# Performance work log

Hardware: AMD Instinct MI355X
Metric: run time of the kernel (lower is better)

## Reference

```python
import jax, jax.numpy as jnp
import numpy as np

B, S, D, H = 128, 512, 512, 4
DH = D // H

def setup_inputs() -> dict:
    key = jax.random.key(0)
    ks = jax.random.split(key, 12)
    s = 1.0 / np.sqrt(D)
    inp = {
        "x": jax.random.normal(ks[0], (B, S, D), dtype=jnp.float32),
        "Wi": jax.random.uniform(ks[1], (D, D), jnp.float32, -s, s),
        "bi": jnp.zeros((D,), jnp.float32),
        "Wq": jax.random.uniform(ks[2], (D, D), jnp.float32, -s, s),
        "bq": jnp.zeros((D,), jnp.float32),
        "Wk": jax.random.uniform(ks[3], (D, D), jnp.float32, -s, s),
        "bk": jnp.zeros((D,), jnp.float32),
        "Wv": jax.random.uniform(ks[4], (D, D), jnp.float32, -s, s),
        "bv": jnp.zeros((D,), jnp.float32),
        "Wo": jax.random.uniform(ks[5], (D, D), jnp.float32, -s, s),
        "bo": jnp.zeros((D,), jnp.float32),
        "data_lens": jax.random.randint(ks[6], (B,), 1, S + 1, dtype=jnp.int32),
    }
    return inp


def _forward(x, Wi, bi, Wq, bq, Wk, bk, Wv, bv, Wo, bo, data_lens):
    # fc_i applied to the whole sequence up front
    xf = x @ Wi + bi                      # [B, S, D]
    h0 = xf[:, 0, :]                      # initial state = fc_i(x)[:, 0]
    scale = 1.0 / jnp.sqrt(jnp.asarray(DH, xf.dtype))

    def step(h, x_t):
        # h: [B, D] previous state (acts as key and value, kv_len == 1)
        # x_t: [B, D] current input (query)
        q = (x_t @ Wq + bq).reshape(B, H, DH)
        k = (h @ Wk + bk).reshape(B, H, DH)
        v = (h @ Wv + bv).reshape(B, H, DH)
        scores = jnp.sum(q * k, axis=-1, keepdims=True) * scale   # [B, H, 1]
        w = jax.nn.softmax(scores, axis=-1)                       # == 1 (single key)
        attn = (w * v).reshape(B, D)
        h_new = attn @ Wo + bo + x_t                              # residual
        return h_new, h_new

    xs = jnp.transpose(xf, (1, 0, 2))     # [S, B, D]
    _, outs = jax.lax.scan(step, h0, xs)  # [S, B, D]
    outputs = jnp.transpose(outs, (1, 0, 2))                      # [B, S, D]

    idx = (data_lens.astype(jnp.int32) - 1)[:, None, None]        # [B,1,1]
    final_state = jnp.take_along_axis(outputs, idx, axis=1)[:, 0, :]
    return outputs, final_state


def reference(x, Wi, bi, Wq, bq, Wk, bk, Wv, bv, Wo, bo, data_lens):
    return _forward(x, Wi, bi, Wq, bq, Wk, bk, Wv, bv, Wo, bo, data_lens)
```

## Files before the change

### kernel.cpp

```cpp
#include <hip/hip_runtime.h>
#include <hip/hip_bf16.h>

typedef __hip_bfloat16 bf16;
typedef __attribute__((ext_vector_type(8))) short short8;
typedef __attribute__((ext_vector_type(4))) float f32x4;

#define S_LEN 512
#define DIM   512
#define BATCH 128
#define ROWS  (BATCH * S_LEN)

__device__ inline unsigned short f2bu(float f){
    bf16 h = __float2bfloat16(f);
    return *reinterpret_cast<unsigned short*>(&h);
}
__device__ inline float ld_in(const void* p, size_t i, int f32){
    return f32 ? ((const float*)p)[i] : __bfloat162float(((const bf16*)p)[i]);
}

__global__ void detect_dtype(const unsigned int* __restrict__ x, int* __restrict__ flag)
{
    __shared__ int cnt;
    if (threadIdx.x == 0) cnt = 0;
    __syncthreads();
    int loc = 0;
    for (int i = threadIdx.x; i < 8192; i += 256)
        if (((x[i] >> 7) & 0xFFu) == 0xFFu) loc++;
    atomicAdd(&cnt, loc);
    __syncthreads();
    if (threadIdx.x == 0) *flag = (cnt > 0) ? 1 : 0;
}

__global__ void conv_tr(const void* __restrict__ in, bf16* __restrict__ outp,
                        const int* __restrict__ flagp)
{
    const int f32 = *flagp;
    __shared__ unsigned short tile[32][33];
    const int bx = blockIdx.x, by = blockIdx.y;
    const int tx = threadIdx.x, ty = threadIdx.y;
    #pragma unroll
    for (int j = 0; j < 32; j += 8)
        tile[ty + j][tx] = f2bu(ld_in(in, (size_t)(by*32 + ty + j)*DIM + bx*32 + tx, f32));
    __syncthreads();
    #pragma unroll
    for (int j = 0; j < 32; j += 8) {
        unsigned short u = tile[tx][ty + j];
        outp[(size_t)(bx*32 + ty + j)*DIM + by*32 + tx] = *reinterpret_cast<bf16*>(&u);
    }
}

__global__ void conv_cp(const void* __restrict__ in, bf16* __restrict__ outp,
                        const int* __restrict__ flagp)
{
    const int f32 = *flagp;
    const size_t i = (size_t)blockIdx.x*256 + threadIdx.x;
    outp[i] = __float2bfloat16(ld_in(in, i, f32));
}

__global__ void cvec_kernel(const bf16* __restrict__ WoT, const void* __restrict__ bv,
                            const void* __restrict__ bo, const void* __restrict__ bi,
                            const int* __restrict__ flagp,
                            float* __restrict__ dvec, float* __restrict__ bvec)
{
    const int f32 = *flagp;
    const int n = threadIdx.x;
    float acc = 0.f;
    for (int k = 0; k < DIM; ++k)
        acc += ld_in(bv, k, f32) * __bfloat162float(WoT[(size_t)n*DIM + k]);
    const float dd = acc + ld_in(bo, n, f32);
    dvec[n] = dd;
    bvec[n] = dd + ld_in(bi, n, f32);
}

#define TILE_PROLOGUE                                                          \
    __shared__ __align__(16) unsigned short As[128][72];                       \
    __shared__ __align__(16) unsigned short Bs[128][72];                       \
    const int tid  = threadIdx.x;                                              \
    const int lane = tid & 63;                                                 \
    const int wave = tid >> 6;                                                 \
    const int wm = (wave & 1) * 64;                                            \
    const int wn = (wave >> 1) * 64;                                           \
    const int cn = lane & 15;                                                  \
    const int quad = lane >> 4;                                                \
    f32x4 acc[4][4];                                                           \
    _Pragma("unroll")                                                          \
    for (int i = 0; i < 4; ++i)                                                \
        _Pragma("unroll")                                                      \
        for (int j = 0; j < 4; ++j) acc[i][j] = (f32x4){0.f,0.f,0.f,0.f};

#define TILE_MFMA                                                              \
        __syncthreads();                                                       \
        _Pragma("unroll")                                                      \
        for (int ks = 0; ks < 64; ks += 32) {                                  \
            short8 af[4], bfr[4];                                              \
            const int koff = ks + quad*8;                                      \
            _Pragma("unroll")                                                  \
            for (int i = 0; i < 4; ++i) af[i]  = *(const short8*)&As[wm + i*16 + cn][koff]; \
            _Pragma("unroll")                                                  \
            for (int j = 0; j < 4; ++j) bfr[j] = *(const short8*)&Bs[wn + j*16 + cn][koff]; \
            _Pragma("unroll")                                                  \
            for (int i = 0; i < 4; ++i)                                        \
                _Pragma("unroll")                                              \
                for (int j = 0; j < 4; ++j)                                    \
                    acc[i][j] = __builtin_amdgcn_mfma_f32_16x16x32_bf16(af[i], bfr[j], acc[i][j], 0, 0, 0); \
        }                                                                      \
        __syncthreads();

#define STAGE_B(Bt, C0)                                                        \
        {                                                                      \
            int r = tid >> 3; const int c = (tid & 7) * 8;                     \
            _Pragma("unroll")                                                  \
            for (int p = 0; p < 4; ++p, r += 32) {                             \
                uint4 v = *(const uint4*)((Bt) + (size_t)((C0) + r)*DIM + k0 + c); \
                *(uint4*)&Bs[r][c] = v;                                        \
            }                                                                  \
        }

#define STAGE_A_IN(SRC, BASE)                                                  \
                if (f32) {                                                     \
                    const float* sp = (const float*)(SRC) + (BASE);            \
                    float4 a = *(const float4*)sp;                             \
                    float4 b = *(const float4*)(sp + 4);                       \
                    __align__(16) unsigned short w[8];                         \
                    w[0]=f2bu(a.x); w[1]=f2bu(a.y); w[2]=f2bu(a.z); w[3]=f2bu(a.w); \
                    w[4]=f2bu(b.x); w[5]=f2bu(b.y); w[6]=f2bu(b.z); w[7]=f2bu(b.w); \
                    *(uint4*)&As[r][c] = *(const uint4*)w;                     \
                } else {                                                       \
                    *(uint4*)&As[r][c] = *(const uint4*)((const bf16*)(SRC) + (BASE)); \
                }

__global__ __launch_bounds__(256) void gemm_sq(const bf16* __restrict__ A,
        const bf16* __restrict__ Btm, bf16* __restrict__ Pout, bf16* __restrict__ Tout)
{
    TILE_PROLOGUE
    const int R0 = blockIdx.y * 128;
    const int C0 = blockIdx.x * 128;
    for (int k0 = 0; k0 < DIM; k0 += 64) {
        {
            int r = tid >> 3; const int c = (tid & 7) * 8;
            #pragma unroll
            for (int p = 0; p < 4; ++p, r += 32)
                *(uint4*)&As[r][c] = *(const uint4*)(A + (size_t)(R0 + r)*DIM + k0 + c);
        }
        STAGE_B(Btm, C0)
        TILE_MFMA
    }
    #pragma unroll
    for (int i = 0; i < 4; ++i) {
        const int rowb = R0 + wm + i*16 + quad*4;
        #pragma unroll
        for (int j = 0; j < 4; ++j) {
            const int cc = C0 + wn + j*16 + cn;
            #pragma unroll
            for (int rr = 0; rr < 4; ++rr) {
                const float v = acc[i][j][rr];
                Pout[(size_t)(rowb + rr)*DIM + cc] = __float2bfloat16(v);
                Tout[(size_t)cc*DIM + rowb + rr]  = __float2bfloat16(v);
            }
        }
    }
}

__global__ __launch_bounds__(256) void gemm_xf_chunk(const void* __restrict__ X,
        size_t eoff, const bf16* __restrict__ WiT, const float* __restrict__ bvec,
        const int* __restrict__ flagp, float* __restrict__ U)
{
    const int f32 = *flagp;
    TILE_PROLOGUE
    const int R0 = blockIdx.y * 128;
    const int C0 = blockIdx.x * 128;
    for (int k0 = 0; k0 < DIM; k0 += 64) {
        {
            int r = tid >> 3; const int c = (tid & 7) * 8;
            #pragma unroll
            for (int p = 0; p < 4; ++p, r += 32) {
                const size_t base = eoff + (size_t)(R0 + r)*DIM + k0 + c;
                STAGE_A_IN(X, base)
            }
        }
        STAGE_B(WiT, C0)
        TILE_MFMA
    }
    #pragma unroll
    for (int i = 0; i < 4; ++i) {
        const int rowb = R0 + wm + i*16 + quad*4;
        #pragma unroll
        for (int j = 0; j < 4; ++j) {
            const int cc = C0 + wn + j*16 + cn;
            const float bb = bvec[cc];
            #pragma unroll
            for (int rr = 0; rr < 4; ++rr)
                U[(size_t)(rowb + rr)*DIM + cc] = acc[i][j][rr] + bb;
        }
    }
}

__global__ __launch_bounds__(256) void gemm_row0(const void* __restrict__ X,
        const bf16* __restrict__ WiT, const float* __restrict__ bvec,
        const int* __restrict__ flagp, float* __restrict__ U0)
{
    const int f32 = *flagp;
    TILE_PROLOGUE
    const int C0 = blockIdx.x * 128;
    for (int k0 = 0; k0 < DIM; k0 += 64) {
        {
            int r = tid >> 3; const int c = (tid & 7) * 8;
            #pragma unroll
            for (int p = 0; p < 4; ++p, r += 32) {
                const size_t base = (size_t)r*S_LEN*DIM + k0 + c;
                STAGE_A_IN(X, base)
            }
        }
        STAGE_B(WiT, C0)
        TILE_MFMA
    }
    #pragma unroll
    for (int i = 0; i < 4; ++i) {
        const int rowb = wm + i*16 + quad*4;
        #pragma unroll
        for (int j = 0; j < 4; ++j) {
            const int cc = C0 + wn + j*16 + cn;
            const float bb = bvec[cc];
            #pragma unroll
            for (int rr = 0; rr < 4; ++rr)
                U0[(size_t)(rowb + rr)*DIM + cc] = acc[i][j][rr] + bb;
        }
    }
}

__global__ __launch_bounds__(256) void gemm_v0(const float* __restrict__ U0,
        const bf16* __restrict__ T0, const float* __restrict__ dvec, float* __restrict__ V0)
{
    TILE_PROLOGUE
    const int C0 = blockIdx.x * 128;
    for (int k0 = 0; k0 < DIM; k0 += 64) {
        {
            int r = tid >> 3; const int c = (tid & 7) * 8;
            #pragma unroll
            for (int p = 0; p < 4; ++p, r += 32) {
                __align__(16) unsigned short w[8];
                #pragma unroll
                for (int q = 0; q < 8; ++q)
                    w[q] = f2bu(U0[(size_t)r*DIM + k0 + c + q] - dvec[k0 + c + q]);
                *(uint4*)&As[r][c] = *(const uint4*)w;
            }
        }
        STAGE_B(T0, C0)
        TILE_MFMA
    }
    #pragma unroll
    for (int i = 0; i < 4; ++i) {
        const int rowb = wm + i*16 + quad*4;
        #pragma unroll
        for (int j = 0; j < 4; ++j) {
            const int cc = C0 + wn + j*16 + cn;
            #pragma unroll
            for (int rr = 0; rr < 4; ++rr) {
                const size_t off = (size_t)(rowb + rr)*DIM + cc;
                V0[off] = acc[i][j][rr] + U0[off];
            }
        }
    }
}

template<bool TO_OUT>
__global__ __launch_bounds__(256) void gemm_level(const float* __restrict__ yin,
        void* __restrict__ yout, size_t eoff, const bf16* __restrict__ Bt,
        const float* __restrict__ dvec, const float* __restrict__ V0c,
        const int* __restrict__ flagp, const int shift, const int mode)
{
    const int f32 = *flagp;
    TILE_PROLOGUE
    const int R0 = blockIdx.y * 128;
    const int C0 = blockIdx.x * 128;
    for (int k0 = 0; k0 < DIM; k0 += 64) {
        {
            int r = tid >> 3; const int c = (tid & 7) * 8;
            #pragma unroll
            for (int p = 0; p < 4; ++p, r += 32) {
                const int row = R0 + r;
                const int t = row & (S_LEN - 1);
                __align__(16) unsigned short w[8];
                if (mode && t == 1) {
                    const float* vp = V0c + (size_t)(row >> 9)*DIM + k0 + c;
                    #pragma unroll
                    for (int q = 0; q < 8; ++q) w[q] = f2bu(vp[q]);
                } else if (mode && t == 0) {
                    const float* sp = yin + (size_t)row*DIM + k0 + c;
                    #pragma unroll
                    for (int q = 0; q < 8; ++q) w[q] = f2bu(sp[q] - dvec[k0 + c + q]);
                } else if (t >= shift) {
                    const float* sp = yin + (size_t)(row - shift)*DIM + k0 + c;
                    #pragma unroll
                    for (int q = 0; q < 8; ++q) w[q] = f2bu(sp[q]);
                } else {
                    #pragma unroll
                    for (int q = 0; q < 8; ++q) w[q] = 0;
                }
                *(uint4*)&As[r][c] = *(const uint4*)w;
            }
        }
        STAGE_B(Bt, C0)
        TILE_MFMA
    }
    #pragma unroll
    for (int i = 0; i < 4; ++i) {
        const int rowb = R0 + wm + i*16 + quad*4;
        #pragma unroll
        for (int j = 0; j < 4; ++j) {
            const int cc = C0 + wn + j*16 + cn;
            #pragma unroll
            for (int rr = 0; rr < 4; ++rr) {
                const size_t off = (size_t)(rowb + rr)*DIM + cc;
                const float v = acc[i][j][rr] + yin[off];
                if (TO_OUT) {
                    if (f32) ((float*)yout)[eoff + off] = v;
                    else     ((bf16*)yout)[eoff + off] = __float2bfloat16(v);
                } else {
                    ((float*)yout)[off] = v;
                }
            }
        }
    }
}

__global__ void gather_final(void* __restrict__ out, const int* __restrict__ lens,
                             const int* __restrict__ flagp)
{
    const int f32 = *flagp;
    const int idx = blockIdx.x * 256 + threadIdx.x;
    const int b = idx >> 9, n = idx & 511;
    int L = lens[b];
    if (L < 1) L = 1;
    if (L > S_LEN) L = S_LEN;
    const size_t src = ((size_t)b*S_LEN + (L - 1))*DIM + n;
    const size_t dst = (size_t)ROWS*DIM + idx;
    if (f32) ((float*)out)[dst] = ((const float*)out)[src];
    else     ((bf16*)out)[dst]  = ((const bf16*)out)[src];
}

extern "C" void kernel_launch(void* const* d_in, const int* in_sizes, int n_in,
                              void* d_out, int out_size, void* d_ws, size_t ws_size,
                              hipStream_t stream)
{
    const void* X  = d_in[0];
    const void* Wi = d_in[1];
    const void* bi = d_in[2];
    const void* Wv = d_in[7];
    const void* bv = d_in[8];
    const void* Wo = d_in[9];
    const void* bo = d_in[10];
    const int* lens = (const int*)d_in[11];
    char* ws = (char*)d_ws;

    const size_t MATB = (size_t)DIM * DIM * sizeof(bf16);
    bf16* WiT = (bf16*)(ws + 0*MATB);
    bf16* WoT = (bf16*)(ws + 1*MATB);
    bf16* Wvb = (bf16*)(ws + 2*MATB);
    bf16* S2  = (bf16*)(ws + 3*MATB);
    bf16* S3  = (bf16*)(ws + 4*MATB);
    bf16* T0  = (bf16*)(ws + 5*MATB);
    bf16* T1  = (bf16*)(ws + 6*MATB);
    bf16* T2  = (bf16*)(ws + 7*MATB);
    bf16* T3  = (bf16*)(ws + 8*MATB);
    float* dvec = (float*)(ws + 9*MATB);
    float* bvec = dvec + DIM;
    int*   flag = (int*)(bvec + DIM);
    float* U0   = (float*)(flag + 64);
    float* V0   = U0 + (size_t)BATCH*DIM;
    char*  dyn  = (char*)(V0 + (size_t)BATCH*DIM);
    const size_t fixed = (size_t)(dyn - ws);
    const size_t avail = ws_size > fixed ? ws_size - fixed : 0;

    int CR = 512;
    for (int cr = 65536; cr >= 512; cr >>= 1)
        if ((size_t)2*cr*DIM*4 <= avail) { CR = cr; break; }

    detect_dtype<<<1, 256, 0, stream>>>((const unsigned int*)X, flag);
    conv_tr<<<dim3(16,16), dim3(32,8), 0, stream>>>(Wi, WiT, flag);
    conv_tr<<<dim3(16,16), dim3(32,8), 0, stream>>>(Wo, WoT, flag);
    conv_cp<<<1024, 256, 0, stream>>>(Wv, Wvb, flag);
    cvec_kernel<<<1, DIM, 0, stream>>>(WoT, bv, bo, bi, flag, dvec, bvec);
    gemm_sq<<<dim3(4,4), 256, 0, stream>>>(Wvb, WoT, S2, T0);
    gemm_sq<<<dim3(4,4), 256, 0, stream>>>(S2, T0, S3, T1);
    gemm_sq<<<dim3(4,4), 256, 0, stream>>>(S3, T1, S2, T2);
    gemm_sq<<<dim3(4,4), 256, 0, stream>>>(S2, T2, S3, T3);
    gemm_row0<<<dim3(4,1), 256, 0, stream>>>(X, WiT, bvec, flag, U0);
    gemm_v0<<<dim3(4,1), 256, 0, stream>>>(U0, T0, dvec, V0);

    float* bufA = (float*)dyn;
    float* bufB = bufA + (size_t)CR*DIM;
    const int NC = ROWS / CR;
    const int RT = CR / 128;
    for (int c = 0; c < NC; ++c) {
        const size_t eoff = (size_t)c*CR*DIM;
        const float* V0c = V0 + (size_t)(c*(CR/S_LEN))*DIM;
        gemm_xf_chunk<<<dim3(4,RT), 256, 0, stream>>>(X, eoff, WiT, bvec, flag, bufA);
        gemm_level<false><<<dim3(4,RT), 256, 0, stream>>>(bufA, bufB, 0, T0, dvec, V0c, flag, 1, 1);
        gemm_level<false><<<dim3(4,RT), 256, 0, stream>>>(bufB, bufA, 0, T1, dvec, V0c, flag, 2, 0);
        gemm_level<false><<<dim3(4,RT), 256, 0, stream>>>(bufA, bufB, 0, T2, dvec, V0c, flag, 4, 0);
        gemm_level<true ><<<dim3(4,RT), 256, 0, stream>>>(bufB, d_out, eoff, T3, dvec, V0c, flag, 8, 0);
    }
    gather_final<<<256, 256, 0, stream>>>(d_out, lens, flag);
}
```

Measured before the change: 1.144 ms.

## Stage GEMM operands as bf16 via direct global-to-LDS loads

Replaces the per-level GEMM kernels with a unified gemm_big. Its A operand is a bf16 copy written by the previous level, and both tiles are staged through global_load_lds 16-byte loads into unpadded LDS. Input x is converted to bf16 by a separate pass, row-0/row-1 special cases are precomputed into small bf16 arrays, and block indices are swizzled for L2 locality. This removes the per-element fp32 load, convert and store to LDS in the inner loop, at the cost of extra bf16 writes per level and unpadded LDS rows that may cause bank conflicts. cvec is also parallelised with wave reductions.

```diff
diff --git a/kernel.cpp b/kernel.cpp
--- a/kernel.cpp
+++ b/kernel.cpp
@@ -16,6 +16,12 @@
 }
 __device__ inline float ld_in(const void* p, size_t i, int f32){
     return f32 ? ((const float*)p)[i] : __bfloat162float(((const bf16*)p)[i]);
+}
+
+typedef __attribute__((address_space(1))) const unsigned int gu32;
+typedef __attribute__((address_space(3))) unsigned int lu32;
+__device__ __forceinline__ void gld16(const void* g, void* l){
+    __builtin_amdgcn_global_load_lds((gu32*)g, (lu32*)l, 16, 0, 0);
 }
 
 __global__ void detect_dtype(const unsigned int* __restrict__ x, int* __restrict__ flag)
@@ -57,19 +63,53 @@
     outp[i] = __float2bfloat16(ld_in(in, i, f32));
 }
 
+__global__ void conv_x(const void* __restrict__ X, size_t eoff, bf16* __restrict__ xb,
+                       const int* __restrict__ flagp)
+{
+    const int f32 = *flagp;
+    const size_t i = ((size_t)blockIdx.x*256 + threadIdx.x)*8;
+    if (f32) {
+        const float* p = (const float*)X + eoff + i;
+        float4 a = *(const float4*)p;
+        float4 b = *(const float4*)(p + 4);
+        __align__(16) unsigned short wv[8];
+        wv[0]=f2bu(a.x); wv[1]=f2bu(a.y); wv[2]=f2bu(a.z); wv[3]=f2bu(a.w);
+        wv[4]=f2bu(b.x); wv[5]=f2bu(b.y); wv[6]=f2bu(b.z); wv[7]=f2bu(b.w);
+        *(uint4*)(xb + i) = *(const uint4*)wv;
+    } else {
+        *(uint4*)(xb + i) = *(const uint4*)((const bf16*)X + eoff + i);
+    }
+}
+
 __global__ void cvec_kernel(const bf16* __restrict__ WoT, const void* __restrict__ bv,
                             const void* __restrict__ bo, const void* __restrict__ bi,
                             const int* __restrict__ flagp,
                             float* __restrict__ dvec, float* __restrict__ bvec)
 {
     const int f32 = *flagp;
-    const int n = threadIdx.x;
+    const int n = blockIdx.x * 4 + (threadIdx.x >> 6);
+    const int lane = threadIdx.x & 63;
     float acc = 0.f;
-    for (int k = 0; k < DIM; ++k)
+    for (int k = lane; k < DIM; k += 64)
         acc += ld_in(bv, k, f32) * __bfloat162float(WoT[(size_t)n*DIM + k]);
-    const float dd = acc + ld_in(bo, n, f32);
-    dvec[n] = dd;
-    bvec[n] = dd + ld_in(bi, n, f32);
+    #pragma unroll
+    for (int o = 32; o > 0; o >>= 1) acc += __shfl_down(acc, o, 64);
+    if (lane == 0) {
+        const float dd = acc + ld_in(bo, n, f32);
+        dvec[n] = dd;
+        bvec[n] = dd + ld_in(bi, n, f32);
+    }
+}
+
+__global__ void prep_aux(const float* __restrict__ U0, const float* __restrict__ V0,
+                         const float* __restrict__ dvec,
+                         bf16* __restrict__ A1, bf16* __restrict__ V0b, bf16* __restrict__ Zr)
+{
+    const int idx = blockIdx.x * 256 + threadIdx.x;
+    const int n = idx & 511;
+    A1[idx]  = __float2bfloat16(U0[idx] - dvec[n]);
+    V0b[idx] = __float2bfloat16(V0[idx]);
+    if (idx < 512) Zr[idx] = __float2bfloat16(0.f);
 }
 
 #define TILE_PROLOGUE                                                          \
@@ -161,40 +201,6 @@
     }
 }
 
-__global__ __launch_bounds__(256) void gemm_xf_chunk(const void* __restrict__ X,
-        size_t eoff, const bf16* __restrict__ WiT, const float* __restrict__ bvec,
-        const int* __restrict__ flagp, float* __restrict__ U)
-{
-    const int f32 = *flagp;
-    TILE_PROLOGUE
-    const int R0 = blockIdx.y * 128;
-    const int C0 = blockIdx.x * 128;
-    for (int k0 = 0; k0 < DIM; k0 += 64) {
-        {
-            int r = tid >> 3; const int c = (tid & 7) * 8;
-            #pragma unroll
-            for (int p = 0; p < 4; ++p, r += 32) {
-                const size_t base = eoff + (size_t)(R0 + r)*DIM + k0 + c;
-                STAGE_A_IN(X, base)
-            }
-        }
-        STAGE_B(WiT, C0)
-        TILE_MFMA
-    }
-    #pragma unroll
-    for (int i = 0; i < 4; ++i) {
-        const int rowb = R0 + wm + i*16 + quad*4;
-        #pragma unroll
-        for (int j = 0; j < 4; ++j) {
-            const int cc = C0 + wn + j*16 + cn;
-            const float bb = bvec[cc];
-            #pragma unroll
-            for (int rr = 0; rr < 4; ++rr)
-                U[(size_t)(rowb + rr)*DIM + cc] = acc[i][j][rr] + bb;
-        }
-    }
-}
-
 __global__ __launch_bounds__(256) void gemm_row0(const void* __restrict__ X,
         const bf16* __restrict__ WiT, const float* __restrict__ bvec,
         const int* __restrict__ flagp, float* __restrict__ U0)
@@ -263,46 +269,86 @@
     }
 }
 
-template<bool TO_OUT>
-__global__ __launch_bounds__(256) void gemm_level(const float* __restrict__ yin,
-        void* __restrict__ yout, size_t eoff, const bf16* __restrict__ Bt,
-        const float* __restrict__ dvec, const float* __restrict__ V0c,
-        const int* __restrict__ flagp, const int shift, const int mode)
-{
-    const int f32 = *flagp;
-    TILE_PROLOGUE
-    const int R0 = blockIdx.y * 128;
-    const int C0 = blockIdx.x * 128;
+template<int MODE, bool TO_OUT>
+__global__ __launch_bounds__(256) void gemm_big(
+        const bf16* __restrict__ Abf, const bf16* __restrict__ A1,
+        const bf16* __restrict__ V0b, const bf16* __restrict__ Zr,
+        const bf16* __restrict__ Bt,  const float* __restrict__ Rf,
+        float* __restrict__ Of, bf16* __restrict__ Ob,
+        void* __restrict__ Oout, size_t eoff, const int* __restrict__ flagp,
+        const int shift)
+{
+    __shared__ __align__(16) unsigned short As[128*64];
+    __shared__ __align__(16) unsigned short Bs[128*64];
+    const int tid  = threadIdx.x;
+    const int lane = tid & 63;
+    const int w    = tid >> 6;
+    const int nb = gridDim.x;
+    const int p0 = blockIdx.x;
+    const int L  = (p0 & 7) * (nb >> 3) + (p0 >> 3);
+    const int bx = L & 3, by = L >> 2;
+    const int R0 = by * 128, C0 = bx * 128;
+    const int wm = (w & 1) * 64;
+    const int wn = (w >> 1) * 64;
+    const int cn = lane & 15;
+    const int quad = lane >> 4;
+    f32x4 acc[4][4];
+    #pragma unroll
+    for (int i = 0; i < 4; ++i)
+        #pragma unroll
+        for (int j = 0; j < 4; ++j) acc[i][j] = (f32x4){0.f,0.f,0.f,0.f};
+
+    const int lr = lane >> 3;
+    const int lc = (lane & 7) * 8;
+    const bf16* ab[4];
+    const bf16* bb[4];
+    #pragma unroll
+    for (int p = 0; p < 4; ++p) {
+        const int seg  = w*4 + p;
+        const int r    = seg*8 + lr;
+        const int grow = R0 + r;
+        const bf16* a;
+        if (MODE == 2) {
+            a = Abf + (size_t)grow*DIM;
+        } else if (MODE == 1) {
+            const int t = grow & (S_LEN - 1);
+            if      (t == 0) a = A1  + (size_t)(grow >> 9)*DIM;
+            else if (t == 1) a = V0b + (size_t)(grow >> 9)*DIM;
+            else             a = Abf + (size_t)(grow - 1)*DIM;
+        } else {
+            const int t = grow & (S_LEN - 1);
+            a = (t >= shift) ? (Abf + (size_t)(grow - shift)*DIM) : Zr;
+        }
+        ab[p] = a + lc;
+        bb[p] = Bt + (size_t)(C0 + r)*DIM + lc;
+    }
+
     for (int k0 = 0; k0 < DIM; k0 += 64) {
-        {
-            int r = tid >> 3; const int c = (tid & 7) * 8;
-            #pragma unroll
-            for (int p = 0; p < 4; ++p, r += 32) {
-                const int row = R0 + r;
-                const int t = row & (S_LEN - 1);
-                __align__(16) unsigned short w[8];
-                if (mode && t == 1) {
-                    const float* vp = V0c + (size_t)(row >> 9)*DIM + k0 + c;
-                    #pragma unroll
-                    for (int q = 0; q < 8; ++q) w[q] = f2bu(vp[q]);
-                } else if (mode && t == 0) {
-                    const float* sp = yin + (size_t)row*DIM + k0 + c;
-                    #pragma unroll
-                    for (int q = 0; q < 8; ++q) w[q] = f2bu(sp[q] - dvec[k0 + c + q]);
-                } else if (t >= shift) {
-                    const float* sp = yin + (size_t)(row - shift)*DIM + k0 + c;
-                    #pragma unroll
-                    for (int q = 0; q < 8; ++q) w[q] = f2bu(sp[q]);
-                } else {
-                    #pragma unroll
-                    for (int q = 0; q < 8; ++q) w[q] = 0;
-                }
-                *(uint4*)&As[r][c] = *(const uint4*)w;
-            }
-        }
-        STAGE_B(Bt, C0)
-        TILE_MFMA
-    }
+        #pragma unroll
+        for (int p = 0; p < 4; ++p) {
+            const int seg = w*4 + p;
+            gld16(ab[p] + k0, &As[seg*512]);
+            gld16(bb[p] + k0, &Bs[seg*512]);
+        }
+        __syncthreads();
+        #pragma unroll
+        for (int ks = 0; ks < 64; ks += 32) {
+            short8 af[4], bfr[4];
+            const int koff = ks + quad*8;
+            #pragma unroll
+            for (int i = 0; i < 4; ++i) af[i]  = *(const short8*)&As[(wm + i*16 + cn)*64 + koff];
+            #pragma unroll
+            for (int j = 0; j < 4; ++j) bfr[j] = *(const short8*)&Bs[(wn + j*16 + cn)*64 + koff];
+            #pragma unroll
+            for (int i = 0; i < 4; ++i)
+                #pragma unroll
+                for (int j = 0; j < 4; ++j)
+                    acc[i][j] = __builtin_amdgcn_mfma_f32_16x16x32_bf16(af[i], bfr[j], acc[i][j], 0, 0, 0);
+        }
+        __syncthreads();
+    }
+
+    const int f32o = TO_OUT ? *flagp : 0;
     #pragma unroll
     for (int i = 0; i < 4; ++i) {
         const int rowb = R0 + wm + i*16 + quad*4;
@@ -312,12 +358,14 @@
             #pragma unroll
             for (int rr = 0; rr < 4; ++rr) {
                 const size_t off = (size_t)(rowb + rr)*DIM + cc;
-                const float v = acc[i][j][rr] + yin[off];
+                const float res = (MODE == 2) ? Rf[cc] : Rf[off];
+                const float v = acc[i][j][rr] + res;
                 if (TO_OUT) {
-                    if (f32) ((float*)yout)[eoff + off] = v;
-                    else     ((bf16*)yout)[eoff + off] = __float2bfloat16(v);
+                    if (f32o) ((float*)Oout)[eoff + off] = v;
+                    else      ((bf16*)Oout)[eoff + off]  = __float2bfloat16(v);
                 } else {
-                    ((float*)yout)[off] = v;
+                    Of[off] = v;
+                    Ob[off] = __float2bfloat16(v);
                 }
             }
         }
@@ -363,43 +411,59 @@
     bf16* T1  = (bf16*)(ws + 6*MATB);
     bf16* T2  = (bf16*)(ws + 7*MATB);
     bf16* T3  = (bf16*)(ws + 8*MATB);
-    float* dvec = (float*)(ws + 9*MATB);
-    float* bvec = dvec + DIM;
-    int*   flag = (int*)(bvec + DIM);
-    float* U0   = (float*)(flag + 64);
-    float* V0   = U0 + (size_t)BATCH*DIM;
-    char*  dyn  = (char*)(V0 + (size_t)BATCH*DIM);
-    const size_t fixed = (size_t)(dyn - ws);
-    const size_t avail = ws_size > fixed ? ws_size - fixed : 0;
+    size_t off = 9*MATB;
+    float* dvec = (float*)(ws + off); off += 2048;
+    float* bvec = (float*)(ws + off); off += 2048;
+    int*   flag = (int*)  (ws + off); off += 256;
+    float* U0   = (float*)(ws + off); off += (size_t)BATCH*DIM*4;
+    float* V0   = (float*)(ws + off); off += (size_t)BATCH*DIM*4;
+    bf16*  A1   = (bf16*) (ws + off); off += (size_t)BATCH*DIM*2;
+    bf16*  V0b  = (bf16*) (ws + off); off += (size_t)BATCH*DIM*2;
+    bf16*  Zr   = (bf16*) (ws + off); off += 1024;
+    off = (off + 1023) & ~(size_t)1023;
+    char* dyn = ws + off;
+    const size_t avail = ws_size > off ? ws_size - off : 0;
 
     int CR = 512;
-    for (int cr = 65536; cr >= 512; cr >>= 1)
-        if ((size_t)2*cr*DIM*4 <= avail) { CR = cr; break; }
+    for (long cr = 65536; cr >= 512; cr >>= 1)
+        if ((size_t)cr * 7168 <= avail) { CR = (int)cr; break; }
+
+    bf16*  xbf = (bf16*) dyn;
+    float* Uf  = (float*)(dyn + (size_t)CR*1024);
+    bf16*  Ub  = (bf16*) (dyn + (size_t)CR*3072);
+    float* Vf  = (float*)(dyn + (size_t)CR*4096);
+    bf16*  Vb  = (bf16*) (dyn + (size_t)CR*6144);
 
     detect_dtype<<<1, 256, 0, stream>>>((const unsigned int*)X, flag);
     conv_tr<<<dim3(16,16), dim3(32,8), 0, stream>>>(Wi, WiT, flag);
     conv_tr<<<dim3(16,16), dim3(32,8), 0, stream>>>(Wo, WoT, flag);
     conv_cp<<<1024, 256, 0, stream>>>(Wv, Wvb, flag);
-    cvec_kernel<<<1, DIM, 0, stream>>>(WoT, bv, bo, bi, flag, dvec, bvec);
+    cvec_kernel<<<128, 256, 0, stream>>>(WoT, bv, bo, bi, flag, dvec, bvec);
     gemm_sq<<<dim3(4,4), 256, 0, stream>>>(Wvb, WoT, S2, T0);
     gemm_sq<<<dim3(4,4), 256, 0, stream>>>(S2, T0, S3, T1);
     gemm_sq<<<dim3(4,4), 256, 0, stream>>>(S3, T1, S2, T2);
     gemm_sq<<<dim3(4,4), 256, 0, stream>>>(S2, T2, S3, T3);
     gemm_row0<<<dim3(4,1), 256, 0, stream>>>(X, WiT, bvec, flag, U0);
     gemm_v0<<<dim3(4,1), 256, 0, stream>>>(U0, T0, dvec, V0);
-
-    float* bufA = (float*)dyn;
-    float* bufB = bufA + (size_t)CR*DIM;
+    prep_aux<<<256, 256, 0, stream>>>(U0, V0, dvec, A1, V0b, Zr);
+
     const int NC = ROWS / CR;
     const int RT = CR / 128;
+    const int nb = 4 * RT;
     for (int c = 0; c < NC; ++c) {
         const size_t eoff = (size_t)c*CR*DIM;
-        const float* V0c = V0 + (size_t)(c*(CR/S_LEN))*DIM;
-        gemm_xf_chunk<<<dim3(4,RT), 256, 0, stream>>>(X, eoff, WiT, bvec, flag, bufA);
-        gemm_level<false><<<dim3(4,RT), 256, 0, stream>>>(bufA, bufB, 0, T0, dvec, V0c, flag, 1, 1);
-        gemm_level<false><<<dim3(4,RT), 256, 0, stream>>>(bufB, bufA, 0, T1, dvec, V0c, flag, 2, 0);
-        gemm_level<false><<<dim3(4,RT), 256, 0, stream>>>(bufA, bufB, 0, T2, dvec, V0c, flag, 4, 0);
-        gemm_level<true ><<<dim3(4,RT), 256, 0, stream>>>(bufB, d_out, eoff, T3, dvec, V0c, flag, 8, 0);
+        const size_t boff = (size_t)(c*(CR/S_LEN))*DIM;
+        conv_x<<<CR/4, 256, 0, stream>>>(X, eoff, xbf, flag);
+        gemm_big<2,false><<<nb, 256, 0, stream>>>(xbf, nullptr, nullptr, Zr,
+                WiT, bvec, Uf, Ub, nullptr, 0, flag, 0);
+        gemm_big<1,false><<<nb, 256, 0, stream>>>(Ub, A1 + boff, V0b + boff, Zr,
+                T0, Uf, Vf, Vb, nullptr, 0, flag, 1);
+        gemm_big<0,false><<<nb, 256, 0, stream>>>(Vb, nullptr, nullptr, Zr,
+                T1, Vf, Uf, Ub, nullptr, 0, flag, 2);
+        gemm_big<0,false><<<nb, 256, 0, stream>>>(Ub, nullptr, nullptr, Zr,
+                T2, Uf, Vf, Vb, nullptr, 0, flag, 4);
+        gemm_big<0,true ><<<nb, 256, 0, stream>>>(Vb, nullptr, nullptr, Zr,
+                T3, Vf, nullptr, nullptr, d_out, eoff, flag, 8);
     }
     gather_final<<<256, 256, 0, stream>>>(d_out, lens, flag);
 }
```

New measurement: 1.029 ms. -10.1%, faster.
